# Optimization experiments

Hardware: AMD Instinct MI355X
Metric: run time of the kernel (lower is better)

Reference implementation:

```python
import math
import jax, jax.numpy as jnp
import numpy as np

T = 4096
D_MODEL = 1024
NUM_HEADS = 16
HEAD_DIM = D_MODEL // NUM_HEADS


def setup_inputs() -> dict:
    key = jax.random.key(0)
    k_x, k_wqkv, k_wproj = jax.random.split(key, 3)
    # match eqx.nn.Linear init scale: U(-1/sqrt(in), 1/sqrt(in)); randn*small works too,
    # but keep magnitudes reasonable so softmax isn't saturated.
    s_in = 1.0 / math.sqrt(D_MODEL)
    x = jax.random.normal(k_x, (T, D_MODEL), dtype=jnp.float32)
    W_qkv = jax.random.normal(k_wqkv, (3 * D_MODEL, D_MODEL), dtype=jnp.float32) * s_in
    b_qkv = jnp.zeros((3 * D_MODEL,), dtype=jnp.float32)
    W_proj = jax.random.normal(k_wproj, (D_MODEL, D_MODEL), dtype=jnp.float32) * s_in
    b_proj = jnp.zeros((D_MODEL,), dtype=jnp.float32)
    return {"x": x, "W_qkv": W_qkv, "b_qkv": b_qkv, "W_proj": W_proj, "b_proj": b_proj}


def reference(x, W_qkv, b_qkv, W_proj, b_proj):
    T_, C = x.shape  # (seq, d_model)
    H, hd = NUM_HEADS, HEAD_DIM
    # c_attn: eqx Linear computes W @ x + b per token -> x @ W.T + b
    qkv = x @ W_qkv.T + b_qkv  # (T, 3C)
    q, k, v = jnp.split(qkv, 3, axis=1)
    # (T, C) -> (H, T, hd)
    q = q.reshape(T_, H, hd).swapaxes(0, 1)
    k = k.reshape(T_, H, hd).swapaxes(0, 1)
    v = v.reshape(T_, H, hd).swapaxes(0, 1)
    scores = jnp.einsum("htd,hsd->hts", q, k) / math.sqrt(hd)  # (H, T, T)
    causal = jnp.tril(jnp.ones((T_, T_), dtype=bool))
    scores = jnp.where(causal, scores, -jnp.inf)
    attn = jax.nn.softmax(scores, axis=-1)
    y = jnp.einsum("hts,hsd->htd", attn, v)  # (H, T, hd)
    y = y.swapaxes(0, 1).reshape(T_, C)
    y = y @ W_proj.T + b_proj
    return y
```

## Files before the change

kernel.cpp:

```cpp
#include <hip/hip_runtime.h>
#include <math.h>
#include <string.h>

#define T_SEQ 4096
#define DM 1024
#define NH 16
#define HD 64

typedef short s8v __attribute__((ext_vector_type(8)));
typedef float f4v __attribute__((ext_vector_type(4)));

__device__ inline unsigned short f2bf(float f) {
    unsigned u; memcpy(&u, &f, 4);
    u = u + 0x7fffu + ((u >> 16) & 1u);
    return (unsigned short)(u >> 16);
}

__device__ inline float bf2f(unsigned short s) {
    unsigned u = (unsigned)s << 16;
    float f; memcpy(&f, &u, 4);
    return f;
}

__device__ inline float exp2fn(float x) {
#if __has_builtin(__builtin_amdgcn_exp2f)
    return __builtin_amdgcn_exp2f(x);
#else
    return exp2f(x);
#endif
}

__device__ inline void gld_lds16(const void* g, void* l) {
    __builtin_amdgcn_global_load_lds(
        (const __attribute__((address_space(1))) void*)g,
        (__attribute__((address_space(3))) void*)l, 16, 0, 0);
}

__global__ __launch_bounds__(256)
void cvt3(const float* __restrict__ i0, unsigned short* __restrict__ o0, int n0,
          const float* __restrict__ i1, unsigned short* __restrict__ o1, int n1,
          const float* __restrict__ i2, unsigned short* __restrict__ o2, int n2) {
    int i = blockIdx.x * 256 + threadIdx.x;
    const float* in; unsigned short* out; int j;
    if (i < n0)           { in = i0; out = o0; j = i; }
    else if (i < n0 + n1) { in = i1; out = o1; j = i - n0; }
    else if (i < n0 + n1 + n2) { in = i2; out = o2; j = i - n0 - n1; }
    else return;
    const float4* p = (const float4*)(in + (size_t)j * 8);
    float4 a = p[0], b = p[1];
    unsigned short o[8] = {f2bf(a.x), f2bf(a.y), f2bf(a.z), f2bf(a.w),
                           f2bf(b.x), f2bf(b.y), f2bf(b.z), f2bf(b.w)};
    uint4 pk; memcpy(&pk, o, 16);
    *(uint4*)(out + (size_t)j * 8) = pk;
}

template<int MODE, int TN>
__global__ __launch_bounds__(256)
void gemm_bt_mfma(const unsigned short* __restrict__ A, const unsigned short* __restrict__ B,
                  const float* __restrict__ bias, void* __restrict__ Cout,
                  unsigned short* __restrict__ qbuf, unsigned short* __restrict__ kbuf2,
                  unsigned short* __restrict__ vT,
                  int M, int N, int K) {
    constexpr int NF = TN / 32;
    __shared__ __align__(16) short As[4096];
    __shared__ __align__(16) short Bs[TN * 32];
    const int tid = threadIdx.x;
    const int w = tid >> 6, lane = tid & 63;
    const int wr = w >> 1, wc = w & 1;
    const int m0 = blockIdx.y * 128, n0 = blockIdx.x * TN;

    const bool doA = (w < 2);
    const bool doStage = doA || ((w & 1) * 64 < TN);
    const unsigned short* src = doA ? A : B;
    const int rbase = (doA ? m0 : n0) + (w & 1) * 64;
    const unsigned short* gsrc = src + (size_t)(rbase + (lane & 15)) * K + ((lane >> 4) * 8);
    short* ldst = (doA ? As : Bs) + ((w & 1) * 4) * 512;

    f4v acc[4][NF];
    #pragma unroll
    for (int i = 0; i < 4; ++i)
        #pragma unroll
        for (int j = 0; j < NF; ++j) acc[i][j] = (f4v){0.f, 0.f, 0.f, 0.f};

    for (int k0 = 0; k0 < K; k0 += 32) {
        __syncthreads();
        if (doStage) {
            #pragma unroll
            for (int i = 0; i < 4; ++i)
                gld_lds16(gsrc + (size_t)(i * 16) * K + k0, ldst + i * 512);
        }
        __syncthreads();

        s8v af[4], bf[NF];
        #pragma unroll
        for (int i = 0; i < 4; ++i) af[i] = *(const s8v*)&As[((wr * 4 + i) * 64 + lane) * 8];
        #pragma unroll
        for (int j = 0; j < NF; ++j) bf[j] = *(const s8v*)&Bs[((wc * NF + j) * 64 + lane) * 8];
        #pragma unroll
        for (int i = 0; i < 4; ++i)
            #pragma unroll
            for (int j = 0; j < NF; ++j)
                acc[i][j] = __builtin_amdgcn_mfma_f32_16x16x32_bf16(af[i], bf[j], acc[i][j], 0, 0, 0);
    }

    const int l15 = lane & 15, quad = lane >> 4;
    float bj[NF];
    #pragma unroll
    for (int j = 0; j < NF; ++j) bj[j] = bias[n0 + wc * (TN / 2) + j * 16 + l15];

    if (MODE == 2 && n0 >= 2 * DM) {
        const int tile = (m0 + wr * 64) >> 6;
        const int hh = ((n0 - 2 * DM) >> 6) + wc;
        #pragma unroll
        for (int i = 0; i < 4; ++i) {
            #pragma unroll
            for (int j = 0; j < NF; ++j) {
                unsigned short o[4];
                #pragma unroll
                for (int rg = 0; rg < 4; ++rg) o[rg] = f2bf(acc[i][j][rg] + bj[j]);
                unsigned long long pk; memcpy(&pk, o, 8);
                size_t off = (size_t)hh * 262144 + (size_t)tile * 4096
                           + (size_t)((j * 2 + (i >> 1)) * 64 + lane) * 8 + (i & 1) * 4;
                *(unsigned long long*)&vT[off] = pk;
            }
        }
    } else if (MODE == 2) {
        unsigned short* dst = (n0 < DM) ? qbuf : kbuf2;
        const int nb = (n0 < DM) ? n0 : n0 - DM;
        #pragma unroll
        for (int i = 0; i < 4; ++i) {
            #pragma unroll
            for (int rg = 0; rg < 4; ++rg) {
                int row = m0 + wr * 64 + i * 16 + quad * 4 + rg;
                #pragma unroll
                for (int j = 0; j < NF; ++j) {
                    int col = nb + wc * (TN / 2) + j * 16 + l15;
                    dst[(size_t)row * DM + col] = f2bf(acc[i][j][rg] + bj[j]);
                }
            }
        }
    } else {
        #pragma unroll
        for (int i = 0; i < 4; ++i) {
            #pragma unroll
            for (int rg = 0; rg < 4; ++rg) {
                int row = m0 + wr * 64 + i * 16 + quad * 4 + rg;
                #pragma unroll
                for (int j = 0; j < NF; ++j) {
                    int col = n0 + wc * (TN / 2) + j * 16 + l15;
                    ((float*)Cout)[(size_t)row * N + col] = acc[i][j][rg] + bj[j];
                }
            }
        }
    }
}

__device__ __forceinline__ void soft_step(f4v* st, bool diag, int qloc, int quad,
                                          float& lr, s8v& pf0, s8v& pf1) {
    const float C2  = 0.1803368851f;
    const float MC2 = 12.0f * 0.1803368851f;
    float sv[4][4];
    #pragma unroll
    for (int kb = 0; kb < 4; ++kb)
        #pragma unroll
        for (int rg = 0; rg < 4; ++rg) {
            float s = st[kb][rg];
            if (diag && (kb * 16 + quad * 4 + rg > qloc)) s = -3.0e38f;
            float t = exp2fn(fmaf(s, C2, -MC2));
            sv[kb][rg] = t;
            lr += t;
        }
    int pk[4][2];
    #pragma unroll
    for (int kb = 0; kb < 4; ++kb) {
        unsigned u0 = __float_as_uint(sv[kb][0]) + 0x8000u;
        unsigned u1 = __float_as_uint(sv[kb][1]) + 0x8000u;
        unsigned u2 = __float_as_uint(sv[kb][2]) + 0x8000u;
        unsigned u3 = __float_as_uint(sv[kb][3]) + 0x8000u;
        pk[kb][0] = (int)__builtin_amdgcn_perm(u1, u0, 0x07060302);
        pk[kb][1] = (int)__builtin_amdgcn_perm(u3, u2, 0x07060302);
    }
    int4 a = {pk[0][0], pk[0][1], pk[1][0], pk[1][1]};
    int4 b = {pk[2][0], pk[2][1], pk[3][0], pk[3][1]};
    memcpy(&pf0, &a, 16);
    memcpy(&pf1, &b, 16);
}

__global__ __launch_bounds__(256, 3)
void attn_mfma7(const unsigned short* __restrict__ qb,
                const unsigned short* __restrict__ kbf,
                const unsigned short* __restrict__ vT,
                unsigned short* __restrict__ y0,
                unsigned short* __restrict__ y1,
                unsigned short* __restrict__ y2,
                float* __restrict__ lsum) {
    const int b = blockIdx.x;
    const int par = b % 3;
    const int idx = b / 3;
    const int h = idx & 15, a = idx >> 4;
    const int tid = threadIdx.x;
    const int w = tid >> 6, lane = tid & 63;
    const int quad = lane >> 4, l15 = lane & 15;
    const int cq = h * HD;
    unsigned short* ypar = (par == 0) ? y0 : (par == 1) ? y1 : y2;
    float* lpar = lsum + ((size_t)par * NH + h) * T_SEQ;
    const unsigned short* vbase = vT + (size_t)h * 262144;

    __shared__ short KB[2][4096];
    __shared__ short VTs[2][4096];
    __shared__ short QB[8192];

    for (int ph = 0; ph < 2; ++ph) {
        const int qt = ph ? (31 - a) : a;
        const int q0 = qt * 128;
        const int kmax = 2 * qt + 1;
        const int nk = (kmax >= par) ? (kmax - par) / 3 + 1 : 0;
        const int kt0 = par * 64;

        __syncthreads();
        #pragma unroll
        for (int rr = 0; rr < 4; ++rr) {
            int ch = rr * 256 + tid;
            int qg = ch >> 7, hf = (ch >> 6) & 1, ln = ch & 63;
            gld_lds16(qb + (size_t)(q0 + qg * 16 + (ln & 15)) * DM + cq + hf * 32 + ((ln >> 4) << 3),
                      &QB[(ch & ~63) * 8]);
        }
        if (nk > 0) {
            #pragma unroll
            for (int rr = 0; rr < 2; ++rr) {
                int ch = rr * 256 + tid;
                int blk = ch >> 7, hf = (ch >> 6) & 1, ln = ch & 63;
                gld_lds16(kbf + (size_t)(kt0 + blk * 16 + (ln & 15)) * DM + cq + hf * 32 + ((ln >> 4) << 3),
                          &KB[0][(ch & ~63) * 8]);
                gld_lds16(vbase + (size_t)(kt0 >> 6) * 4096 + (size_t)ch * 8,
                          &VTs[0][(ch & ~63) * 8]);
            }
        }
        __syncthreads();

        s8v qf[2][2];
        #pragma unroll
        for (int g = 0; g < 2; ++g)
            #pragma unroll
            for (int hf = 0; hf < 2; ++hf)
                qf[g][hf] = *(const s8v*)&QB[((((g * 4 + w) * 2 + hf) * 64) + lane) * 8];

        f4v O0[4], O1[4];
        #pragma unroll
        for (int ob = 0; ob < 4; ++ob) {
            O0[ob] = (f4v){0.f, 0.f, 0.f, 0.f};
            O1[ob] = (f4v){0.f, 0.f, 0.f, 0.f};
        }
        float lr0 = 0.f, lr1 = 0.f;

        for (int i = 0; i < nk; ++i) {
            const int kt = par + 3 * i;
            const int p = i & 1;
            const bool g0a = (kt <= 2 * qt);
            const bool m0 = (kt == 2 * qt);
            const bool m1 = (kt == 2 * qt + 1);
            if (i < nk - 1) {
                const int k1 = kt0 + (i + 1) * 192;
                #pragma unroll
                for (int rr = 0; rr < 2; ++rr) {
                    int ch = rr * 256 + tid;
                    int blk = ch >> 7, hf = (ch >> 6) & 1, ln = ch & 63;
                    gld_lds16(kbf + (size_t)(k1 + blk * 16 + (ln & 15)) * DM + cq
                                  + hf * 32 + ((ln >> 4) << 3),
                              &KB[p ^ 1][(ch & ~63) * 8]);
                    gld_lds16(vbase + (size_t)(k1 >> 6) * 4096 + (size_t)ch * 8,
                              &VTs[p ^ 1][(ch & ~63) * 8]);
                }
            }

            f4v st0[4], st1[4];
            #pragma unroll
            for (int kb = 0; kb < 4; ++kb) {
                s8v k0f = *(const s8v*)&KB[p][((kb * 2 + 0) * 64 + lane) * 8];
                s8v k1f = *(const s8v*)&KB[p][((kb * 2 + 1) * 64 + lane) * 8];
                f4v c1 = (f4v){0.f, 0.f, 0.f, 0.f};
                c1 = __builtin_amdgcn_mfma_f32_16x16x32_bf16(k0f, qf[1][0], c1, 0, 0, 0);
                c1 = __builtin_amdgcn_mfma_f32_16x16x32_bf16(k1f, qf[1][1], c1, 0, 0, 0);
                st1[kb] = c1;
                if (g0a) {
                    f4v c0 = (f4v){0.f, 0.f, 0.f, 0.f};
                    c0 = __builtin_amdgcn_mfma_f32_16x16x32_bf16(k0f, qf[0][0], c0, 0, 0, 0);
                    c0 = __builtin_amdgcn_mfma_f32_16x16x32_bf16(k1f, qf[0][1], c0, 0, 0, 0);
                    st0[kb] = c0;
                }
            }

            s8v pf10, pf11, pf00, pf01;
            soft_step(st1, m1, w * 16 + l15, quad, lr1, pf10, pf11);
            if (g0a) soft_step(st0, m0, w * 16 + l15, quad, lr0, pf00, pf01);

            #pragma unroll
            for (int ob = 0; ob < 4; ++ob) {
                s8v v0f = *(const s8v*)&VTs[p][((ob * 2 + 0) * 64 + lane) * 8];
                s8v v1f = *(const s8v*)&VTs[p][((ob * 2 + 1) * 64 + lane) * 8];
                O1[ob] = __builtin_amdgcn_mfma_f32_16x16x32_bf16(v0f, pf10, O1[ob], 0, 0, 0);
                O1[ob] = __builtin_amdgcn_mfma_f32_16x16x32_bf16(v1f, pf11, O1[ob], 0, 0, 0);
                if (g0a) {
                    O0[ob] = __builtin_amdgcn_mfma_f32_16x16x32_bf16(v0f, pf00, O0[ob], 0, 0, 0);
                    O0[ob] = __builtin_amdgcn_mfma_f32_16x16x32_bf16(v1f, pf01, O0[ob], 0, 0, 0);
                }
            }
            __syncthreads();
        }

        lr0 += __shfl_xor(lr0, 16); lr0 += __shfl_xor(lr0, 32);
        lr1 += __shfl_xor(lr1, 16); lr1 += __shfl_xor(lr1, 32);
        #pragma unroll
        for (int g = 0; g < 2; ++g) {
            const f4v* O = g ? O1 : O0;
            int qrow = q0 + g * 64 + w * 16 + l15;
            size_t ybase = (size_t)qrow * DM + cq;
            #pragma unroll
            for (int ob = 0; ob < 4; ++ob) {
                unsigned short o[4];
                #pragma unroll
                for (int rg = 0; rg < 4; ++rg) o[rg] = f2bf(O[ob][rg]);
                unsigned long long pk; memcpy(&pk, o, 8);
                *(unsigned long long*)&ypar[ybase + ob * 16 + quad * 4] = pk;
            }
            if (quad == 0) lpar[qrow] = g ? lr1 : lr0;
        }
    }
}

__global__ __launch_bounds__(256)
void attn_combine3(const unsigned short* __restrict__ y0,
                   const unsigned short* __restrict__ y1,
                   const unsigned short* __restrict__ y2,
                   const float* __restrict__ lsum,
                   unsigned short* __restrict__ yout) {
    int i = blockIdx.x * 256 + threadIdx.x;
    int t = i >> 7, d8 = i & 127;
    int h = d8 >> 3;
    float l = lsum[(size_t)h * T_SEQ + t]
            + lsum[((size_t)NH + h) * T_SEQ + t]
            + lsum[((size_t)2 * NH + h) * T_SEQ + t];
    float inv = 1.f / l;
    size_t off = (size_t)t * DM + d8 * 8;
    uint4 ua = *(const uint4*)(y0 + off);
    uint4 ub = *(const uint4*)(y1 + off);
    uint4 uc = *(const uint4*)(y2 + off);
    const unsigned short* pa = (const unsigned short*)&ua;
    const unsigned short* pb = (const unsigned short*)&ub;
    const unsigned short* pc = (const unsigned short*)&uc;
    unsigned short o[8];
    #pragma unroll
    for (int k = 0; k < 8; ++k)
        o[k] = f2bf((bf2f(pa[k]) + bf2f(pb[k]) + bf2f(pc[k])) * inv);
    uint4 pk; memcpy(&pk, o, 16);
    *(uint4*)(yout + off) = pk;
}

extern "C" void kernel_launch(void* const* d_in, const int* in_sizes, int n_in,
                              void* d_out, int out_size, void* d_ws, size_t ws_size,
                              hipStream_t stream) {
    const float* x     = (const float*)d_in[0];
    const float* Wqkv  = (const float*)d_in[1];
    const float* bqkv  = (const float*)d_in[2];
    const float* Wproj = (const float*)d_in[3];
    const float* bproj = (const float*)d_in[4];
    float* out = (float*)d_out;

    char* ws = (char*)d_ws;
    unsigned short* qbuf  = (unsigned short*)(ws);
    unsigned short* kbuf  = (unsigned short*)(ws + ( 8u << 20));
    unsigned short* vTb   = (unsigned short*)(ws + (16u << 20));
    unsigned short* yattb = (unsigned short*)(ws + (24u << 20));
    unsigned short* wprjb = (unsigned short*)(ws + (32u << 20));
    float*          lsum  = (float*)         (ws + (34u << 20));
    unsigned short* xb    = (unsigned short*)(ws + (35u << 20));
    unsigned short* wqkvb = (unsigned short*)(ws + (43u << 20));
    unsigned short* y0p   = (unsigned short*)(ws + (35u << 20));
    unsigned short* y1p   = (unsigned short*)(ws + (43u << 20));
    unsigned short* y2p   = (unsigned short*)(ws + (51u << 20));

    dim3 blk(256);
    {
        int n0 = T_SEQ * DM / 8, n1 = 3 * DM * DM / 8, n2 = DM * DM / 8;
        cvt3<<<dim3((n0 + n1 + n2 + 255) / 256), blk, 0, stream>>>(
            x, xb, n0, Wqkv, wqkvb, n1, Wproj, wprjb, n2);
    }
    gemm_bt_mfma<2, 128><<<dim3(3 * DM / 128, T_SEQ / 128), blk, 0, stream>>>(
        xb, wqkvb, bqkv, nullptr, qbuf, kbuf, vTb, T_SEQ, 3 * DM, DM);
    attn_mfma7<<<dim3(768), blk, 0, stream>>>(qbuf, kbuf, vTb, y0p, y1p, y2p, lsum);
    attn_combine3<<<dim3(T_SEQ * DM / 8 / 256), blk, 0, stream>>>(y0p, y1p, y2p, lsum, yattb);
    gemm_bt_mfma<0, 64><<<dim3(DM / 64, T_SEQ / 128), blk, 0, stream>>>(
        yattb, wprjb, bproj, out, nullptr, nullptr, nullptr, T_SEQ, DM, DM);
}
```

Before: 218.5 us.

## Split attention KV range four ways, load Q directly to registers

The causal attention kernel now splits each query tile's key range across 4 interleaved partitions instead of 3. That gives 1024 blocks with a 4-blocks-per-CU launch bound. The Q tile is no longer staged in shared memory; each lane loads its Q fragments straight from global memory, which frees LDS so more blocks fit per CU. K/V prefetch addresses are precomputed once and advanced by a fixed stride each iteration. The bf16 packing of softmax probabilities now truncates instead of rounding, and the combine kernel adds a fourth partial buffer, which adds extra memory traffic in the combine step.

```diff
diff --git a/kernel.cpp b/kernel.cpp
--- a/kernel.cpp
+++ b/kernel.cpp
@@ -173,12 +173,10 @@
     int pk[4][2];
     #pragma unroll
     for (int kb = 0; kb < 4; ++kb) {
-        unsigned u0 = __float_as_uint(sv[kb][0]) + 0x8000u;
-        unsigned u1 = __float_as_uint(sv[kb][1]) + 0x8000u;
-        unsigned u2 = __float_as_uint(sv[kb][2]) + 0x8000u;
-        unsigned u3 = __float_as_uint(sv[kb][3]) + 0x8000u;
-        pk[kb][0] = (int)__builtin_amdgcn_perm(u1, u0, 0x07060302);
-        pk[kb][1] = (int)__builtin_amdgcn_perm(u3, u2, 0x07060302);
+        pk[kb][0] = (int)__builtin_amdgcn_perm(__float_as_uint(sv[kb][1]),
+                                               __float_as_uint(sv[kb][0]), 0x07060302);
+        pk[kb][1] = (int)__builtin_amdgcn_perm(__float_as_uint(sv[kb][3]),
+                                               __float_as_uint(sv[kb][2]), 0x07060302);
     }
     int4 a = {pk[0][0], pk[0][1], pk[1][0], pk[1][1]};
     int4 b = {pk[2][0], pk[2][1], pk[3][0], pk[3][1]};
@@ -186,64 +184,69 @@
     memcpy(&pf1, &b, 16);
 }
 
-__global__ __launch_bounds__(256, 3)
-void attn_mfma7(const unsigned short* __restrict__ qb,
+__global__ __launch_bounds__(256, 4)
+void attn_mfma8(const unsigned short* __restrict__ qb,
                 const unsigned short* __restrict__ kbf,
                 const unsigned short* __restrict__ vT,
                 unsigned short* __restrict__ y0,
                 unsigned short* __restrict__ y1,
                 unsigned short* __restrict__ y2,
+                unsigned short* __restrict__ y3,
                 float* __restrict__ lsum) {
     const int b = blockIdx.x;
-    const int par = b % 3;
-    const int idx = b / 3;
+    const int par = b & 3;
+    const int idx = b >> 2;
     const int h = idx & 15, a = idx >> 4;
     const int tid = threadIdx.x;
     const int w = tid >> 6, lane = tid & 63;
     const int quad = lane >> 4, l15 = lane & 15;
     const int cq = h * HD;
-    unsigned short* ypar = (par == 0) ? y0 : (par == 1) ? y1 : y2;
+    unsigned short* ypar = (par == 0) ? y0 : (par == 1) ? y1 : (par == 2) ? y2 : y3;
     float* lpar = lsum + ((size_t)par * NH + h) * T_SEQ;
     const unsigned short* vbase = vT + (size_t)h * 262144;
 
     __shared__ short KB[2][4096];
     __shared__ short VTs[2][4096];
-    __shared__ short QB[8192];
+
+    const int kt0 = par * 64;
+    const int c0 = tid, c1 = 256 + tid;
+    const unsigned short* kb0_base = kbf + (size_t)(kt0 + (c0 >> 7) * 16 + (c0 & 15)) * DM
+                                   + cq + ((c0 >> 6) & 1) * 32 + (((c0 >> 4) & 3) << 3);
+    const unsigned short* kb1_base = kbf + (size_t)(kt0 + (c1 >> 7) * 16 + (c1 & 15)) * DM
+                                   + cq + ((c1 >> 6) & 1) * 32 + (((c1 >> 4) & 3) << 3);
+    const unsigned short* vb0_base = vbase + (size_t)(kt0 >> 6) * 4096 + (size_t)c0 * 8;
+    const unsigned short* vb1_base = vbase + (size_t)(kt0 >> 6) * 4096 + (size_t)c1 * 8;
+    const size_t KS = (size_t)256 * DM;
+    const size_t VS = (size_t)4 * 4096;
+    short* ldsK[2][2] = {{&KB[0][(c0 & ~63) * 8], &KB[0][((c1 & ~63) & 511) * 8 + 2048 * ((c1 >> 8) & 0)]},
+                         {&KB[1][(c0 & ~63) * 8], nullptr}};
+    (void)ldsK;
 
     for (int ph = 0; ph < 2; ++ph) {
         const int qt = ph ? (31 - a) : a;
         const int q0 = qt * 128;
         const int kmax = 2 * qt + 1;
-        const int nk = (kmax >= par) ? (kmax - par) / 3 + 1 : 0;
-        const int kt0 = par * 64;
+        const int nk = (kmax >= par) ? (kmax - par) / 4 + 1 : 0;
 
         __syncthreads();
-        #pragma unroll
-        for (int rr = 0; rr < 4; ++rr) {
-            int ch = rr * 256 + tid;
-            int qg = ch >> 7, hf = (ch >> 6) & 1, ln = ch & 63;
-            gld_lds16(qb + (size_t)(q0 + qg * 16 + (ln & 15)) * DM + cq + hf * 32 + ((ln >> 4) << 3),
-                      &QB[(ch & ~63) * 8]);
-        }
+        const unsigned short* gk0 = kb0_base;
+        const unsigned short* gk1 = kb1_base;
+        const unsigned short* gv0 = vb0_base;
+        const unsigned short* gv1 = vb1_base;
         if (nk > 0) {
-            #pragma unroll
-            for (int rr = 0; rr < 2; ++rr) {
-                int ch = rr * 256 + tid;
-                int blk = ch >> 7, hf = (ch >> 6) & 1, ln = ch & 63;
-                gld_lds16(kbf + (size_t)(kt0 + blk * 16 + (ln & 15)) * DM + cq + hf * 32 + ((ln >> 4) << 3),
-                          &KB[0][(ch & ~63) * 8]);
-                gld_lds16(vbase + (size_t)(kt0 >> 6) * 4096 + (size_t)ch * 8,
-                          &VTs[0][(ch & ~63) * 8]);
-            }
-        }
+            gld_lds16(gk0, &KB[0][(c0 & ~63) * 8]);
+            gld_lds16(gk1, &KB[0][(c1 & ~63) * 8]);
+            gld_lds16(gv0, &VTs[0][(c0 & ~63) * 8]);
+            gld_lds16(gv1, &VTs[0][(c1 & ~63) * 8]);
+        }
+        s8v qf[2][2];
+        #pragma unroll
+        for (int g = 0; g < 2; ++g)
+            #pragma unroll
+            for (int hf = 0; hf < 2; ++hf)
+                qf[g][hf] = *(const s8v*)&qb[(size_t)(q0 + (g * 4 + w) * 16 + l15) * DM
+                                             + cq + hf * 32 + quad * 8];
         __syncthreads();
-
-        s8v qf[2][2];
-        #pragma unroll
-        for (int g = 0; g < 2; ++g)
-            #pragma unroll
-            for (int hf = 0; hf < 2; ++hf)
-                qf[g][hf] = *(const s8v*)&QB[((((g * 4 + w) * 2 + hf) * 64) + lane) * 8];
 
         f4v O0[4], O1[4];
         #pragma unroll
@@ -254,23 +257,19 @@
         float lr0 = 0.f, lr1 = 0.f;
 
         for (int i = 0; i < nk; ++i) {
-            const int kt = par + 3 * i;
+            const int kt = par + 4 * i;
             const int p = i & 1;
             const bool g0a = (kt <= 2 * qt);
             const bool m0 = (kt == 2 * qt);
             const bool m1 = (kt == 2 * qt + 1);
             if (i < nk - 1) {
-                const int k1 = kt0 + (i + 1) * 192;
-                #pragma unroll
-                for (int rr = 0; rr < 2; ++rr) {
-                    int ch = rr * 256 + tid;
-                    int blk = ch >> 7, hf = (ch >> 6) & 1, ln = ch & 63;
-                    gld_lds16(kbf + (size_t)(k1 + blk * 16 + (ln & 15)) * DM + cq
-                                  + hf * 32 + ((ln >> 4) << 3),
-                              &KB[p ^ 1][(ch & ~63) * 8]);
-                    gld_lds16(vbase + (size_t)(k1 >> 6) * 4096 + (size_t)ch * 8,
-                              &VTs[p ^ 1][(ch & ~63) * 8]);
-                }
+                gk0 += KS; gk1 += KS; gv0 += VS; gv1 += VS;
+                short* dK = KB[p ^ 1];
+                short* dV = VTs[p ^ 1];
+                gld_lds16(gk0, &dK[(c0 & ~63) * 8]);
+                gld_lds16(gk1, &dK[(c1 & ~63) * 8]);
+                gld_lds16(gv0, &dV[(c0 & ~63) * 8]);
+                gld_lds16(gv1, &dV[(c1 & ~63) * 8]);
             }
 
             f4v st0[4], st1[4];
@@ -278,15 +277,15 @@
             for (int kb = 0; kb < 4; ++kb) {
                 s8v k0f = *(const s8v*)&KB[p][((kb * 2 + 0) * 64 + lane) * 8];
                 s8v k1f = *(const s8v*)&KB[p][((kb * 2 + 1) * 64 + lane) * 8];
-                f4v c1 = (f4v){0.f, 0.f, 0.f, 0.f};
-                c1 = __builtin_amdgcn_mfma_f32_16x16x32_bf16(k0f, qf[1][0], c1, 0, 0, 0);
-                c1 = __builtin_amdgcn_mfma_f32_16x16x32_bf16(k1f, qf[1][1], c1, 0, 0, 0);
-                st1[kb] = c1;
+                f4v c1v = (f4v){0.f, 0.f, 0.f, 0.f};
+                c1v = __builtin_amdgcn_mfma_f32_16x16x32_bf16(k0f, qf[1][0], c1v, 0, 0, 0);
+                c1v = __builtin_amdgcn_mfma_f32_16x16x32_bf16(k1f, qf[1][1], c1v, 0, 0, 0);
+                st1[kb] = c1v;
                 if (g0a) {
-                    f4v c0 = (f4v){0.f, 0.f, 0.f, 0.f};
-                    c0 = __builtin_amdgcn_mfma_f32_16x16x32_bf16(k0f, qf[0][0], c0, 0, 0, 0);
-                    c0 = __builtin_amdgcn_mfma_f32_16x16x32_bf16(k1f, qf[0][1], c0, 0, 0, 0);
-                    st0[kb] = c0;
+                    f4v c0v = (f4v){0.f, 0.f, 0.f, 0.f};
+                    c0v = __builtin_amdgcn_mfma_f32_16x16x32_bf16(k0f, qf[0][0], c0v, 0, 0, 0);
+                    c0v = __builtin_amdgcn_mfma_f32_16x16x32_bf16(k1f, qf[0][1], c0v, 0, 0, 0);
+                    st0[kb] = c0v;
                 }
             }
 
@@ -329,9 +328,10 @@
 }
 
 __global__ __launch_bounds__(256)
-void attn_combine3(const unsigned short* __restrict__ y0,
+void attn_combine4(const unsigned short* __restrict__ y0,
                    const unsigned short* __restrict__ y1,
                    const unsigned short* __restrict__ y2,
+                   const unsigned short* __restrict__ y3,
                    const float* __restrict__ lsum,
                    unsigned short* __restrict__ yout) {
     int i = blockIdx.x * 256 + threadIdx.x;
@@ -339,19 +339,22 @@
     int h = d8 >> 3;
     float l = lsum[(size_t)h * T_SEQ + t]
             + lsum[((size_t)NH + h) * T_SEQ + t]
-            + lsum[((size_t)2 * NH + h) * T_SEQ + t];
+            + lsum[((size_t)2 * NH + h) * T_SEQ + t]
+            + lsum[((size_t)3 * NH + h) * T_SEQ + t];
     float inv = 1.f / l;
     size_t off = (size_t)t * DM + d8 * 8;
     uint4 ua = *(const uint4*)(y0 + off);
     uint4 ub = *(const uint4*)(y1 + off);
     uint4 uc = *(const uint4*)(y2 + off);
+    uint4 ud = *(const uint4*)(y3 + off);
     const unsigned short* pa = (const unsigned short*)&ua;
     const unsigned short* pb = (const unsigned short*)&ub;
     const unsigned short* pc = (const unsigned short*)&uc;
+    const unsigned short* pd = (const unsigned short*)&ud;
     unsigned short o[8];
     #pragma unroll
     for (int k = 0; k < 8; ++k)
-        o[k] = f2bf((bf2f(pa[k]) + bf2f(pb[k]) + bf2f(pc[k])) * inv);
+        o[k] = f2bf((bf2f(pa[k]) + bf2f(pb[k]) + bf2f(pc[k]) + bf2f(pd[k])) * inv);
     uint4 pk; memcpy(&pk, o, 16);
     *(uint4*)(yout + off) = pk;
 }
@@ -378,6 +381,7 @@
     unsigned short* y0p   = (unsigned short*)(ws + (35u << 20));
     unsigned short* y1p   = (unsigned short*)(ws + (43u << 20));
     unsigned short* y2p   = (unsigned short*)(ws + (51u << 20));
+    unsigned short* y3p   = yattb;
 
     dim3 blk(256);
     {
@@ -387,8 +391,9 @@
     }
     gemm_bt_mfma<2, 128><<<dim3(3 * DM / 128, T_SEQ / 128), blk, 0, stream>>>(
         xb, wqkvb, bqkv, nullptr, qbuf, kbuf, vTb, T_SEQ, 3 * DM, DM);
-    attn_mfma7<<<dim3(768), blk, 0, stream>>>(qbuf, kbuf, vTb, y0p, y1p, y2p, lsum);
-    attn_combine3<<<dim3(T_SEQ * DM / 8 / 256), blk, 0, stream>>>(y0p, y1p, y2p, lsum, yattb);
+    attn_mfma8<<<dim3(1024), blk, 0, stream>>>(qbuf, kbuf, vTb, y0p, y1p, y2p, y3p, lsum);
+    attn_combine4<<<dim3(T_SEQ * DM / 8 / 256), blk, 0, stream>>>(
+        y0p, y1p, y2p, y3p, lsum, yattb);
     gemm_bt_mfma<0, 64><<<dim3(DM / 64, T_SEQ / 128), blk, 0, stream>>>(
         yattb, wprjb, bproj, out, nullptr, nullptr, nullptr, T_SEQ, DM, DM);
 }
```

After: 238.9 us. 9.4% more time.
